# Optimization experiments

Measured on AMD Instinct MI355X. Metric: run time of the kernel, lower is better.

Reference implementation:

```python
import jax, jax.numpy as jnp
import numpy as np

N = 50000          # num nodes
E = 800000         # num edges (avg degree 16)
R = 8              # num relations
IN = 128
H0 = 256
H1 = 64


def _w(key, shape, fan_in):
    return jax.random.normal(key, shape, dtype=jnp.float32) * (1.0 / np.sqrt(fan_in))


def setup_inputs() -> dict:
    key = jax.random.key(0)
    ks = jax.random.split(key, 16)
    x = jax.random.normal(ks[0], (N, IN), dtype=jnp.float32)
    edge_index = jax.random.randint(ks[1], (2, E), 0, N, dtype=jnp.int64)
    edge_type = jax.random.randint(ks[2], (E,), 0, R, dtype=jnp.int64)
    return {
        "x": x,
        "edge_index": edge_index,
        "edge_type": edge_type,
        # RGCNConv params: per-relation weights [R, in, out], root weight [in, out], bias [out]
        "W1": _w(ks[3], (R, IN, H0), IN), "root1": _w(ks[4], (IN, H0), IN), "b1": jnp.zeros((H0,), jnp.float32),
        "W2": _w(ks[5], (R, H0, H0), H0), "root2": _w(ks[6], (H0, H0), H0), "b2": jnp.zeros((H0,), jnp.float32),
        "W3": _w(ks[7], (R, H0, H0), H0), "root3": _w(ks[8], (H0, H0), H0), "b3": jnp.zeros((H0,), jnp.float32),
        "W4": _w(ks[9], (R, H0, H1), H0), "root4": _w(ks[10], (H0, H1), H0), "b4": jnp.zeros((H1,), jnp.float32),
    }


def rgcn_layer(x, edge_index, edge_type, W, root, bias):
    """PyG RGCNConv: out_i = x_i @ root + sum_r (1/|N_r(i)|) sum_{j in N_r(i)} x_j @ W_r + bias.
    Aggregation is linear, so aggregate source features per (relation, dst) first,
    then apply the R small GEMMs — avoids per-edge [E, out] message materialization."""
    src, dst = edge_index[0], edge_index[1]
    seg = edge_type * N + dst                      # combined (relation, dst) segment id
    nseg = R * N
    agg = jax.ops.segment_sum(x[src], seg, num_segments=nseg)          # [R*N, in]
    cnt = jax.ops.segment_sum(jnp.ones((seg.shape[0],), x.dtype), seg, num_segments=nseg)
    agg = agg / jnp.maximum(cnt, 1.0)[:, None]                          # mean per (r, i)
    agg = agg.reshape(R, N, x.shape[1])                                 # [R, N, in]
    return jnp.einsum('rni,rio->no', agg, W) + x @ root + bias


def reference(x, edge_index, edge_type, W1, root1, b1, W2, root2, b2, W3, root3, b3, W4, root4, b4):
    h = jax.nn.relu(rgcn_layer(x, edge_index, edge_type, W1, root1, b1))
    h = jax.nn.relu(rgcn_layer(h, edge_index, edge_type, W2, root2, b2))
    h = jax.nn.relu(rgcn_layer(h, edge_index, edge_type, W3, root3, b3))
    return rgcn_layer(h, edge_index, edge_type, W4, root4, b4)
```

## Files before the change

### kernel.cpp

```cpp
#include <hip/hip_runtime.h>

#define N_NODES 50000
#define N_PAD   50048
#define N_EDGES 800000
#define N_REL   8
#define NSEG    (N_REL * N_NODES)
#define SCAN_NB 391
#define NSTRIPE 391
#define SPX     49

typedef short bf16x8 __attribute__((ext_vector_type(8)));
typedef float f32x4  __attribute__((ext_vector_type(4)));

__device__ __forceinline__ ushort f2bf(float f) {
    union { float f; unsigned u; } c; c.f = f;
    unsigned u = c.u + 0x7fffu + ((c.u >> 16) & 1u);
    return (ushort)(u >> 16);
}
__device__ __forceinline__ void add8(float* s, uint4 v) {
    unsigned u[4] = {v.x, v.y, v.z, v.w};
    #pragma unroll
    for (int k = 0; k < 4; ++k) {
        s[2 * k]     += __uint_as_float(u[k] << 16);
        s[2 * k + 1] += __uint_as_float(u[k] & 0xffff0000u);
    }
}
__device__ __forceinline__ void fma8(float* s, uint4 v, float w) {
    unsigned u[4] = {v.x, v.y, v.z, v.w};
    #pragma unroll
    for (int k = 0; k < 4; ++k) {
        s[2 * k]     = fmaf(__uint_as_float(u[k] << 16),        w, s[2 * k]);
        s[2 * k + 1] = fmaf(__uint_as_float(u[k] & 0xffff0000u), w, s[2 * k + 1]);
    }
}
__device__ __forceinline__ void async16(const ushort* g, ushort* l) {
    __builtin_amdgcn_global_load_lds((const __attribute__((address_space(1))) void*)g,
                                     (__attribute__((address_space(3))) void*)l, 16, 0, 0);
}


__global__ void count_edges(const int* __restrict__ dst, const int* __restrict__ et,
                            int* __restrict__ cnt) {
    int e = blockIdx.x * 256 + threadIdx.x;
    if (e < N_EDGES) atomicAdd(&cnt[dst[e] * N_REL + et[e]], 1);
}

__global__ __launch_bounds__(256) void scan_pass1(const int* __restrict__ cnt,
                                                  int* __restrict__ sums) {
    __shared__ int sc[256];
    int b = blockIdx.x, t = threadIdx.x;
    int base = b * 1024 + t * 4;
    int v = 0;
    #pragma unroll
    for (int i = 0; i < 4; ++i) { int idx = base + i; if (idx < NSEG) v += cnt[idx]; }
    sc[t] = v; __syncthreads();
    for (int off = 1; off < 256; off <<= 1) {
        int x = (t >= off) ? sc[t - off] : 0;
        __syncthreads(); sc[t] += x; __syncthreads();
    }
    if (t == 255) sums[b] = sc[255];
}

__global__ __launch_bounds__(512) void scan_pass2(int* __restrict__ sums, int nb) {
    __shared__ int sc[512];
    int t = threadIdx.x;
    int v = (t < nb) ? sums[t] : 0;
    sc[t] = v; __syncthreads();
    for (int off = 1; off < 512; off <<= 1) {
        int x = (t >= off) ? sc[t - off] : 0;
        __syncthreads(); sc[t] += x; __syncthreads();
    }
    if (t < nb) sums[t] = sc[t] - v;
}

__global__ __launch_bounds__(256) void scan_pass3(const int* __restrict__ cnt,
                                                  const int* __restrict__ sums,
                                                  int* __restrict__ row_ptr) {
    __shared__ int sc[256];
    int b = blockIdx.x, t = threadIdx.x;
    int base = b * 1024 + t * 4;
    int e[4]; int v = 0;
    #pragma unroll
    for (int i = 0; i < 4; ++i) { int idx = base + i; e[i] = (idx < NSEG) ? cnt[idx] : 0; v += e[i]; }
    sc[t] = v; __syncthreads();
    for (int off = 1; off < 256; off <<= 1) {
        int x = (t >= off) ? sc[t - off] : 0;
        __syncthreads(); sc[t] += x; __syncthreads();
    }
    int run = sums[b] + (sc[t] - v);
    #pragma unroll
    for (int i = 0; i < 4; ++i) {
        int idx = base + i;
        if (idx < NSEG) row_ptr[idx] = run;
        run += e[i];
    }
    if (b == 0 && t == 0) row_ptr[NSEG] = N_EDGES;
}

__global__ void place_edges(const int* __restrict__ src, const int* __restrict__ dst,
                            const int* __restrict__ et, const int* __restrict__ row_ptr,
                            int* __restrict__ cnt, int* __restrict__ sorted) {
    int e = blockIdx.x * 256 + threadIdx.x;
    if (e >= N_EDGES) return;
    int r = et[e];
    int key = dst[e] * N_REL + r;
    int old = atomicSub(&cnt[key], 1);
    int r0 = row_ptr[key];
    int c = row_ptr[key + 1] - r0;
    sorted[r0 + old - 1] = src[e] | (r << 17) | (c << 20);
}


__global__ void convert_weights(const float* __restrict__ W, const float* __restrict__ root,
                                ushort* __restrict__ BT, int K, int O, int NPAD) {
    int idx = blockIdx.x * 256 + threadIdx.x;
    if (idx >= NPAD * K) return;
    int col = idx / K, i = idx % K;
    float v = 0.0f;
    if (col < N_REL * O) {
        int r = col / O, o = col % O;
        v = W[((size_t)r * K + i) * O + o];
    } else if (col < (N_REL + 1) * O) {
        v = root[(size_t)i * O + (col - N_REL * O)];
    }
    BT[idx] = f2bf(v);
}

__global__ void f32_to_bf16(const float* __restrict__ in, ushort* __restrict__ out, int n4) {
    int i = blockIdx.x * 256 + threadIdx.x;
    if (i >= n4) return;
    float4 v = ((const float4*)in)[i];
    ushort4 s; s.x = f2bf(v.x); s.y = f2bf(v.y); s.z = f2bf(v.z); s.w = f2bf(v.w);
    ((ushort4*)out)[i] = s;
}

template<int K, int CTS, int NW>
__global__ __launch_bounds__(256)
void gemm_mfma(const ushort* __restrict__ A, const ushort* __restrict__ BT,
               ushort* __restrict__ Y) {
    const int f = blockIdx.x;
    const int g = f & 7, m = f >> 3;
    const int y = g + 8 * (m / CTS);
    const int ct = m % CTS;
    if (y >= NSTRIPE) return;
    const int row0 = y * 128;
    const int col0 = ct * 128;

    __shared__ ushort SMEM[16384];
    const int t = threadIdx.x;
    const int lane = t & 63;
    const int w = t >> 6;
    const int l16 = lane & 15, q = lane >> 4;
    const int wm = (w & 1) * 64, wn = (w >> 1) * 64;

    const int c0i = w * 64 + lane;
    const int c1i = c0i + 256;
    const int r0i = c0i >> 2, r1i = c1i >> 2;
    const int j0i = (c0i & 3) ^ ((r0i >> 1) & 3);
    const int j1i = (c1i & 3) ^ ((r1i >> 1) & 3);
    const size_t ga0 = (size_t)r0i * K + (size_t)j0i * 8;
    const size_t ga1 = (size_t)r1i * K + (size_t)j1i * 8;
    const ushort* Ab = A + (size_t)row0 * K;
    const ushort* Bb = BT + (size_t)col0 * K;

    const int qx = (q ^ ((l16 >> 1) & 3)) * 8;

    f32x4 acc[4][4] = {};

    auto STAGE = [&](int b, int k0) {
        ushort* As = SMEM + b * 8192;
        ushort* Bs = As + 4096;
        async16(Ab + k0 + ga0, &As[w * 512]);
        async16(Ab + k0 + ga1, &As[(w + 4) * 512]);
        async16(Bb + k0 + ga0, &Bs[w * 512]);
        async16(Bb + k0 + ga1, &Bs[(w + 4) * 512]);
    };
    auto COMPUTE = [&](int b) {
        ushort* As = SMEM + b * 8192;
        ushort* Bs = As + 4096;
        bf16x8 a[4], bb[4];
        #pragma unroll
        for (int i = 0; i < 4; ++i) {
            a[i]  = *(const bf16x8*)&As[(wm + i * 16 + l16) * 32 + qx];
            bb[i] = *(const bf16x8*)&Bs[(wn + i * 16 + l16) * 32 + qx];
        }
        #pragma unroll
        for (int i = 0; i < 4; ++i)
            #pragma unroll
            for (int j = 0; j < 4; ++j)
                acc[i][j] = __builtin_amdgcn_mfma_f32_16x16x32_bf16(a[i], bb[j], acc[i][j], 0, 0, 0);
    };

    constexpr int NSTEP = K / 32;
    STAGE(0, 0);
    __syncthreads();
    #pragma unroll
    for (int s = 0; s < NSTEP; ++s) {
        if (s + 1 < NSTEP) STAGE((s + 1) & 1, 32 * (s + 1));
        COMPUTE(s & 1);
        __syncthreads();
    }

    ushort* Ts = &SMEM[w * 32 * 72];
    const int rr = lane >> 3;
    const int cc = (lane & 7) * 8;
    #pragma unroll
    for (int half = 0; half < 2; ++half) {
        #pragma unroll
        for (int i = 0; i < 2; ++i)
            #pragma unroll
            for (int j = 0; j < 4; ++j)
                #pragma unroll
                for (int r = 0; r < 4; ++r)
                    Ts[(i * 16 + q * 4 + r) * 72 + j * 16 + l16] = f2bf(acc[half * 2 + i][j][r]);
        #pragma unroll
        for (int p = 0; p < 4; ++p) {
            int row = p * 8 + rr;
            uint4 v = *(const uint4*)&Ts[row * 72 + cc];
            *(uint4*)(Y + (size_t)(row0 + wm + half * 32 + row) * NW + col0 + wn + cc) = v;
        }
    }
}

template<int O>
__global__ __launch_bounds__(256)
void gather_kernel(const ushort* __restrict__ Y, int NW,
                   const int* __restrict__ row_ptr, const int* __restrict__ sorted,
                   const float* __restrict__ bias,
                   float* __restrict__ out_f32, ushort* __restrict__ out_bf16, int relu) {
    constexpr int TPN = O / 8;
    int d = blockIdx.x * (256 / TPN) + threadIdx.x / TPN;
    if (d >= N_NODES) return;
    int c0 = (threadIdx.x % TPN) * 8;
    int p0 = row_ptr[d * N_REL];
    int p1 = row_ptr[d * N_REL + N_REL];
    float sum[8] = {};
    add8(sum, *(const uint4*)(Y + (size_t)d * NW + N_REL * O + c0));
    #pragma unroll
    for (int k = 0; k < 8; ++k) sum[k] += bias[c0 + k];
    const ushort* Yc = Y + c0;
    #define EDGE_LD(sx) (*(const uint4*)(Yc + (size_t)((sx) & 0x1FFFF) * NW + ((((sx) >> 17) & 7) * O)))
    #define EDGE_W(sx)  (1.0f / (float)((unsigned)(sx) >> 20))
    int e = p0;
    for (; e + 4 <= p1; e += 4) {
        int s0 = sorted[e], s1 = sorted[e + 1], s2 = sorted[e + 2], s3 = sorted[e + 3];
        uint4 v0 = EDGE_LD(s0);
        uint4 v1 = EDGE_LD(s1);
        uint4 v2 = EDGE_LD(s2);
        uint4 v3 = EDGE_LD(s3);
        fma8(sum, v0, EDGE_W(s0));
        fma8(sum, v1, EDGE_W(s1));
        fma8(sum, v2, EDGE_W(s2));
        fma8(sum, v3, EDGE_W(s3));
    }
    for (; e < p1; ++e) {
        int s = sorted[e];
        uint4 v = EDGE_LD(s);
        fma8(sum, v, EDGE_W(s));
    }
    #undef EDGE_LD
    #undef EDGE_W
    if (relu) {
        #pragma unroll
        for (int k = 0; k < 8; ++k) sum[k] = fmaxf(sum[k], 0.0f);
    }
    if (out_bf16) {
        ushort o[8];
        #pragma unroll
        for (int k = 0; k < 8; ++k) o[k] = f2bf(sum[k]);
        *(uint4*)(out_bf16 + (size_t)d * O + c0) = *(const uint4*)o;
    } else {
        float* p = out_f32 + (size_t)d * O + c0;
        *(float4*)p = make_float4(sum[0], sum[1], sum[2], sum[3]);
        *(float4*)(p + 4) = make_float4(sum[4], sum[5], sum[6], sum[7]);
    }
}


extern "C" void kernel_launch(void* const* d_in, const int* in_sizes, int n_in,
                              void* d_out, int out_size, void* d_ws, size_t ws_size,
                              hipStream_t stream) {
    const float* x  = (const float*)d_in[0];
    const int*   ei = (const int*)d_in[1];
    const int*   et = (const int*)d_in[2];
    const float* W[4]  = {(const float*)d_in[3], (const float*)d_in[6], (const float*)d_in[9],  (const float*)d_in[12]};
    const float* RT[4] = {(const float*)d_in[4], (const float*)d_in[7], (const float*)d_in[10], (const float*)d_in[13]};
    const float* BI[4] = {(const float*)d_in[5], (const float*)d_in[8], (const float*)d_in[11], (const float*)d_in[14]};
    const int KS[4] = {128, 256, 256, 256};
    const int NP[4] = {2304, 2304, 2304, 640};
    const int* src = ei;
    const int* dst = ei + N_EDGES;

    char* ws = (char*)d_ws;
    size_t off = 0;
    auto take = [&](size_t bytes) -> char* {
        char* p = ws + off;
        off = (off + bytes + 255) & ~(size_t)255;
        return p;
    };
    int* row_ptr    = (int*)take((size_t)(NSEG + 1) * 4);
    int* sorted     = (int*)take((size_t)N_EDGES * 4);
    ushort* BTp[4];
    for (int l = 0; l < 4; ++l) BTp[l] = (ushort*)take((size_t)NP[l] * KS[l] * 2);
    ushort* hb = (ushort*)take((size_t)N_PAD * 256 * 2);
    ushort* Yb = (ushort*)take((size_t)N_PAD * 2304 * 2);
    int* cnt  = (int*)Yb;
    int* sums = (int*)((char*)Yb + (size_t)NSEG * 4);

    hipMemsetAsync(cnt, 0, (size_t)NSEG * 4, stream);
    count_edges<<<(N_EDGES + 255) / 256, 256, 0, stream>>>(dst, et, cnt);
    scan_pass1<<<SCAN_NB, 256, 0, stream>>>(cnt, sums);
    scan_pass2<<<1, 512, 0, stream>>>(sums, SCAN_NB);
    scan_pass3<<<SCAN_NB, 256, 0, stream>>>(cnt, sums, row_ptr);
    place_edges<<<(N_EDGES + 255) / 256, 256, 0, stream>>>(src, dst, et, row_ptr, cnt, sorted);

    for (int l = 0; l < 4; ++l) {
        int n = NP[l] * KS[l];
        convert_weights<<<(n + 255) / 256, 256, 0, stream>>>(W[l], RT[l], BTp[l], KS[l],
                                                             l == 3 ? 64 : 256, NP[l]);
    }

    f32_to_bf16<<<(N_NODES * 128 / 4 + 255) / 256, 256, 0, stream>>>(x, hb, N_NODES * 128 / 4);

    const int G18 = 8 * SPX * 18;
    const int G5  = 8 * SPX * 5;
    gemm_mfma<128, 18, 2304><<<G18, 256, 0, stream>>>(hb, BTp[0], Yb);
    gather_kernel<256><<<dim3((N_NODES + 7) / 8), 256, 0, stream>>>(
        Yb, 2304, row_ptr, sorted, BI[0], nullptr, hb, 1);

    gemm_mfma<256, 18, 2304><<<G18, 256, 0, stream>>>(hb, BTp[1], Yb);
    gather_kernel<256><<<dim3((N_NODES + 7) / 8), 256, 0, stream>>>(
        Yb, 2304, row_ptr, sorted, BI[1], nullptr, hb, 1);

    gemm_mfma<256, 18, 2304><<<G18, 256, 0, stream>>>(hb, BTp[2], Yb);
    gather_kernel<256><<<dim3((N_NODES + 7) / 8), 256, 0, stream>>>(
        Yb, 2304, row_ptr, sorted, BI[2], nullptr, hb, 1);

    gemm_mfma<256, 5, 640><<<G5, 256, 0, stream>>>(hb, BTp[3], Yb);
    gather_kernel<64><<<dim3((N_NODES + 31) / 32), 256, 0, stream>>>(
        Yb, 640, row_ptr, sorted, BI[3], (float*)d_out, nullptr, 0);
}
```

Before: 670.0 us.

## Aggregate-then-transform for hidden layers with fused concat-K GEMM and ReLU epilogue

For layers 1-3, the order becomes aggregate-then-transform. A new agg_gather kernel averages source features per (dst, relation) segment into an [N*8, K] buffer. A new rgcn_gemm kernel then multiplies the concatenated [agg_r..., x] rows against a stacked 9K x 256 weight matrix, applying bias and ReLU in its epilogue. This replaces the wide N x 2304 GEMM output plus a gather over that large intermediate, cutting the bytes written and read per layer. The last layer keeps the old transform-then-gather path, and the new path depends on the memory row order matching the dst*8+r segment key.

```diff
diff --git a/kernel.cpp b/kernel.cpp
--- a/kernel.cpp
+++ b/kernel.cpp
@@ -5,9 +5,12 @@
 #define N_EDGES 800000
 #define N_REL   8
 #define NSEG    (N_REL * N_NODES)
+#define NSEG_PAD 400384
 #define SCAN_NB 391
 #define NSTRIPE 391
+#define NSTRIPE64 782
 #define SPX     49
+#define SPX64   98
 
 typedef short bf16x8 __attribute__((ext_vector_type(8)));
 typedef float f32x4  __attribute__((ext_vector_type(4)));
@@ -110,7 +113,6 @@
     sorted[r0 + old - 1] = src[e] | (r << 17) | (c << 20);
 }
 
-
 __global__ void convert_weights(const float* __restrict__ W, const float* __restrict__ root,
                                 ushort* __restrict__ BT, int K, int O, int NPAD) {
     int idx = blockIdx.x * 256 + threadIdx.x;
@@ -126,12 +128,158 @@
     BT[idx] = f2bf(v);
 }
 
+__global__ void convert_weights2(const float* __restrict__ W, const float* __restrict__ root,
+                                 ushort* __restrict__ BT, int K, int O) {
+    int idx = blockIdx.x * 256 + threadIdx.x;
+    if (idx >= O * 9 * K) return;
+    int o = idx / (9 * K), k = idx % (9 * K);
+    float v;
+    if (k < 8 * K) { int r = k / K, i = k % K; v = W[((size_t)r * K + i) * O + o]; }
+    else v = root[(size_t)(k - 8 * K) * O + o];
+    BT[idx] = f2bf(v);
+}
+
 __global__ void f32_to_bf16(const float* __restrict__ in, ushort* __restrict__ out, int n4) {
     int i = blockIdx.x * 256 + threadIdx.x;
     if (i >= n4) return;
     float4 v = ((const float4*)in)[i];
     ushort4 s; s.x = f2bf(v.x); s.y = f2bf(v.y); s.z = f2bf(v.z); s.w = f2bf(v.w);
     ((ushort4*)out)[i] = s;
+}
+
+template<int K>
+__global__ __launch_bounds__(256)
+void agg_gather(const ushort* __restrict__ X, const int* __restrict__ row_ptr,
+                const int* __restrict__ sorted, ushort* __restrict__ AGG) {
+    constexpr int TPN = K / 8;
+    constexpr int SPB = 256 / TPN;
+    const int seg = blockIdx.x * SPB + threadIdx.x / TPN;
+    const int c0 = (threadIdx.x % TPN) * 8;
+    const int p0 = row_ptr[seg], p1 = row_ptr[seg + 1];
+    float sum[8] = {};
+    const ushort* Xc = X + c0;
+    int e = p0;
+    for (; e + 4 <= p1; e += 4) {
+        int s0 = sorted[e] & 0x1FFFF, s1 = sorted[e + 1] & 0x1FFFF;
+        int s2 = sorted[e + 2] & 0x1FFFF, s3 = sorted[e + 3] & 0x1FFFF;
+        uint4 v0 = *(const uint4*)(Xc + (size_t)s0 * K);
+        uint4 v1 = *(const uint4*)(Xc + (size_t)s1 * K);
+        uint4 v2 = *(const uint4*)(Xc + (size_t)s2 * K);
+        uint4 v3 = *(const uint4*)(Xc + (size_t)s3 * K);
+        add8(sum, v0); add8(sum, v1); add8(sum, v2); add8(sum, v3);
+    }
+    for (; e < p1; ++e)
+        add8(sum, *(const uint4*)(Xc + (size_t)(sorted[e] & 0x1FFFF) * K));
+    ushort o[8];
+    if (p1 > p0) {
+        float inv = 1.0f / (float)(p1 - p0);
+        #pragma unroll
+        for (int k = 0; k < 8; ++k) o[k] = f2bf(sum[k] * inv);
+    } else {
+        #pragma unroll
+        for (int k = 0; k < 8; ++k) o[k] = 0;
+    }
+    *(uint4*)(AGG + (size_t)seg * K + c0) = *(const uint4*)o;
+}
+
+template<int K>
+__global__ __launch_bounds__(256)
+void rgcn_gemm(const ushort* __restrict__ AGG, const ushort* __restrict__ X,
+               const ushort* __restrict__ BT, const float* __restrict__ bias,
+               ushort* __restrict__ H) {
+    constexpr int KTOT  = 9 * K;
+    constexpr int NK1   = K / 4;
+    constexpr int NSTEP = NK1 + K / 32;
+
+    const int f = blockIdx.x;
+    const int g = f & 7, m = f >> 3;
+    const int y = g + 8 * (m >> 1);
+    const int ct = m & 1;
+    if (y >= NSTRIPE64) return;
+    const int row0 = y * 64;
+    const int col0 = ct * 128;
+
+    __shared__ ushort SMEM[12288];
+    const int t = threadIdx.x, lane = t & 63, w = t >> 6;
+    const int l16 = lane & 15, q = lane >> 4;
+    const int wm = (w & 1) * 32;
+    const int wn = (w >> 1) * 64;
+    const int qx = (q ^ ((l16 >> 1) & 3)) * 8;
+
+    const int cA = w * 64 + lane;
+    const int rA = cA >> 2;
+    const int jA = (cA & 3) ^ ((rA >> 1) & 3);
+    const size_t gaA = (size_t)rA * (8 * K) + (size_t)jA * 8;
+    const size_t gaX = (size_t)rA * K + (size_t)jA * 8;
+    const int cB1 = cA + 256;
+    const int rB1 = cB1 >> 2;
+    const int jB1 = (cB1 & 3) ^ ((rB1 >> 1) & 3);
+    const size_t gb0 = (size_t)rA * KTOT + (size_t)jA * 8;
+    const size_t gb1 = (size_t)rB1 * KTOT + (size_t)jB1 * 8;
+
+    const ushort* Abase = AGG + (size_t)row0 * (8 * K);
+    const ushort* Xbase = X + (size_t)row0 * K;
+    const ushort* Bbase = BT + (size_t)col0 * KTOT;
+
+    auto STAGE = [&](int b, int s) {
+        ushort* As = SMEM + b * 6144;
+        ushort* Bs = As + 2048;
+        if (s < NK1) async16(Abase + (size_t)s * 32 + gaA, &As[w * 512]);
+        else         async16(Xbase + (size_t)(s - NK1) * 32 + gaX, &As[w * 512]);
+        const ushort* pb = Bbase + (size_t)s * 32;
+        async16(pb + gb0, &Bs[w * 512]);
+        async16(pb + gb1, &Bs[(w + 4) * 512]);
+    };
+
+    f32x4 acc[2][4] = {};
+    auto COMPUTE = [&](int b) {
+        ushort* As = SMEM + b * 6144;
+        ushort* Bs = As + 2048;
+        bf16x8 a[2], bb[4];
+        #pragma unroll
+        for (int i = 0; i < 2; ++i)
+            a[i] = *(const bf16x8*)&As[(wm + i * 16 + l16) * 32 + qx];
+        #pragma unroll
+        for (int j = 0; j < 4; ++j)
+            bb[j] = *(const bf16x8*)&Bs[(wn + j * 16 + l16) * 32 + qx];
+        #pragma unroll
+        for (int i = 0; i < 2; ++i)
+            #pragma unroll
+            for (int j = 0; j < 4; ++j)
+                acc[i][j] = __builtin_amdgcn_mfma_f32_16x16x32_bf16(a[i], bb[j], acc[i][j], 0, 0, 0);
+    };
+
+    STAGE(0, 0);
+    __syncthreads();
+    for (int s = 0; s < NSTEP; s += 2) {
+        STAGE(1, s + 1);
+        COMPUTE(0);
+        __syncthreads();
+        if (s + 2 < NSTEP) STAGE(0, s + 2);
+        COMPUTE(1);
+        __syncthreads();
+    }
+
+    float bj[4];
+    #pragma unroll
+    for (int j = 0; j < 4; ++j) bj[j] = bias[col0 + wn + j * 16 + l16];
+    ushort* Ts = &SMEM[w * 2304];
+    const int rr2 = lane >> 3, cc = (lane & 7) * 8;
+    #pragma unroll
+    for (int i = 0; i < 2; ++i)
+        #pragma unroll
+        for (int j = 0; j < 4; ++j)
+            #pragma unroll
+            for (int r = 0; r < 4; ++r) {
+                float v = fmaxf(acc[i][j][r] + bj[j], 0.0f);
+                Ts[(i * 16 + q * 4 + r) * 72 + j * 16 + l16] = f2bf(v);
+            }
+    #pragma unroll
+    for (int p = 0; p < 4; ++p) {
+        int row = p * 8 + rr2;
+        uint4 v = *(const uint4*)&Ts[row * 72 + cc];
+        *(uint4*)(H + (size_t)(row0 + wm + row) * 256 + col0 + wn + cc) = v;
+    }
 }
 
 template<int K, int CTS, int NW>
@@ -286,8 +434,6 @@
     const float* W[4]  = {(const float*)d_in[3], (const float*)d_in[6], (const float*)d_in[9],  (const float*)d_in[12]};
     const float* RT[4] = {(const float*)d_in[4], (const float*)d_in[7], (const float*)d_in[10], (const float*)d_in[13]};
     const float* BI[4] = {(const float*)d_in[5], (const float*)d_in[8], (const float*)d_in[11], (const float*)d_in[14]};
-    const int KS[4] = {128, 256, 256, 256};
-    const int NP[4] = {2304, 2304, 2304, 640};
     const int* src = ei;
     const int* dst = ei + N_EDGES;
 
@@ -298,14 +444,19 @@
         off = (off + bytes + 255) & ~(size_t)255;
         return p;
     };
-    int* row_ptr    = (int*)take((size_t)(NSEG + 1) * 4);
-    int* sorted     = (int*)take((size_t)N_EDGES * 4);
-    ushort* BTp[4];
-    for (int l = 0; l < 4; ++l) BTp[l] = (ushort*)take((size_t)NP[l] * KS[l] * 2);
-    ushort* hb = (ushort*)take((size_t)N_PAD * 256 * 2);
-    ushort* Yb = (ushort*)take((size_t)N_PAD * 2304 * 2);
-    int* cnt  = (int*)Yb;
-    int* sums = (int*)((char*)Yb + (size_t)NSEG * 4);
+    int* row_ptr = (int*)take((size_t)(NSEG + 1) * 4);
+    int* sorted  = (int*)take((size_t)N_EDGES * 4);
+    ushort* BT1 = (ushort*)take((size_t)256 * 1152 * 2);
+    ushort* BT2 = (ushort*)take((size_t)256 * 2304 * 2);
+    ushort* BT3 = (ushort*)take((size_t)256 * 2304 * 2);
+    ushort* BT4 = (ushort*)take((size_t)640 * 256 * 2);
+    ushort* Ha  = (ushort*)take((size_t)N_PAD * 256 * 2);
+    ushort* Hb  = (ushort*)take((size_t)N_PAD * 256 * 2);
+    ushort* AGG = (ushort*)take((size_t)NSEG_PAD * 256 * 2);
+    int*    cnt  = (int*)AGG;
+    int*    sums = (int*)((char*)AGG + (size_t)(NSEG + 64) * 4);
+    ushort* X0   = (ushort*)((char*)AGG + 104000000);
+    ushort* Y640 = AGG;
 
     hipMemsetAsync(cnt, 0, (size_t)NSEG * 4, stream);
     count_edges<<<(N_EDGES + 255) / 256, 256, 0, stream>>>(dst, et, cnt);
@@ -314,29 +465,25 @@
     scan_pass3<<<SCAN_NB, 256, 0, stream>>>(cnt, sums, row_ptr);
     place_edges<<<(N_EDGES + 255) / 256, 256, 0, stream>>>(src, dst, et, row_ptr, cnt, sorted);
 
-    for (int l = 0; l < 4; ++l) {
-        int n = NP[l] * KS[l];
-        convert_weights<<<(n + 255) / 256, 256, 0, stream>>>(W[l], RT[l], BTp[l], KS[l],
-                                                             l == 3 ? 64 : 256, NP[l]);
-    }
-
-    f32_to_bf16<<<(N_NODES * 128 / 4 + 255) / 256, 256, 0, stream>>>(x, hb, N_NODES * 128 / 4);
-
-    const int G18 = 8 * SPX * 18;
-    const int G5  = 8 * SPX * 5;
-    gemm_mfma<128, 18, 2304><<<G18, 256, 0, stream>>>(hb, BTp[0], Yb);
-    gather_kernel<256><<<dim3((N_NODES + 7) / 8), 256, 0, stream>>>(
-        Yb, 2304, row_ptr, sorted, BI[0], nullptr, hb, 1);
-
-    gemm_mfma<256, 18, 2304><<<G18, 256, 0, stream>>>(hb, BTp[1], Yb);
-    gather_kernel<256><<<dim3((N_NODES + 7) / 8), 256, 0, stream>>>(
-        Yb, 2304, row_ptr, sorted, BI[1], nullptr, hb, 1);
-
-    gemm_mfma<256, 18, 2304><<<G18, 256, 0, stream>>>(hb, BTp[2], Yb);
-    gather_kernel<256><<<dim3((N_NODES + 7) / 8), 256, 0, stream>>>(
-        Yb, 2304, row_ptr, sorted, BI[2], nullptr, hb, 1);
-
-    gemm_mfma<256, 5, 640><<<G5, 256, 0, stream>>>(hb, BTp[3], Yb);
+    convert_weights2<<<(256 * 1152 + 255) / 256, 256, 0, stream>>>(W[0], RT[0], BT1, 128, 256);
+    convert_weights2<<<(256 * 2304 + 255) / 256, 256, 0, stream>>>(W[1], RT[1], BT2, 256, 256);
+    convert_weights2<<<(256 * 2304 + 255) / 256, 256, 0, stream>>>(W[2], RT[2], BT3, 256, 256);
+    convert_weights<<<(640 * 256 + 255) / 256, 256, 0, stream>>>(W[3], RT[3], BT4, 256, 64, 640);
+
+    f32_to_bf16<<<(N_NODES * 128 / 4 + 255) / 256, 256, 0, stream>>>(x, X0, N_NODES * 128 / 4);
+
+    const int GG = 8 * SPX64 * 2;
+    agg_gather<128><<<NSEG / 16, 256, 0, stream>>>(X0, row_ptr, sorted, AGG);
+    rgcn_gemm<128><<<GG, 256, 0, stream>>>(AGG, X0, BT1, BI[0], Ha);
+
+    agg_gather<256><<<NSEG / 8, 256, 0, stream>>>(Ha, row_ptr, sorted, AGG);
+    rgcn_gemm<256><<<GG, 256, 0, stream>>>(AGG, Ha, BT2, BI[1], Hb);
+
+    agg_gather<256><<<NSEG / 8, 256, 0, stream>>>(Hb, row_ptr, sorted, AGG);
+    rgcn_gemm<256><<<GG, 256, 0, stream>>>(AGG, Hb, BT3, BI[2], Ha);
+
+    const int G5 = 8 * SPX * 5;
+    gemm_mfma<256, 5, 640><<<G5, 256, 0, stream>>>(Ha, BT4, Y640);
     gather_kernel<64><<<dim3((N_NODES + 31) / 32), 256, 0, stream>>>(
-        Yb, 640, row_ptr, sorted, BI[3], (float*)d_out, nullptr, 0);
-}
+        Y640, 640, row_ptr, sorted, BI[3], (float*)d_out, nullptr, 0);
+}
```

After: 732.9 us. +9.4%, slower.
